# Performance work log

Hardware: AMD Instinct MI355X
Metric: run time of the kernel (lower is better)

The kernel has to match this reference:

```python
import jax, jax.numpy as jnp
import numpy as np

B, T, I, H, C = 8192, 28, 28, 128, 10


def setup_inputs() -> dict:
    key = jax.random.key(0)
    ks = jax.random.split(key, 7)
    s_ih = 1.0 / np.sqrt(H)
    return {
        "x": jax.random.normal(ks[0], (B, T, I), dtype=jnp.float32),
        "W_ih": jax.random.normal(ks[1], (4 * H, I), dtype=jnp.float32) * s_ih,
        "W_hh": jax.random.normal(ks[2], (4 * H, H), dtype=jnp.float32) * s_ih,
        "b_ih": jax.random.normal(ks[3], (4 * H,), dtype=jnp.float32) * s_ih,
        "b_hh": jax.random.normal(ks[4], (4 * H,), dtype=jnp.float32) * s_ih,
        "W_fc": jax.random.normal(ks[5], (C, H), dtype=jnp.float32) * s_ih,
        "b_fc": jnp.zeros((C,), dtype=jnp.float32),
    }


def reference(x, W_ih, W_hh, b_ih, b_hh, W_fc, b_fc):
    # x: [B, T, I]. PyTorch LSTM gate order: i, f, g, o.
    b = b_ih + b_hh  # [4H]
    # Precompute input projections for all timesteps: [T, B, 4H]
    x_proj = jnp.einsum("bti,gi->tbg", x, W_ih) + b
    h0 = jnp.zeros((x.shape[0], H), dtype=x.dtype)
    c0 = jnp.zeros_like(h0)

    def step(carry, xp_t):
        h, c = carry
        gates = xp_t + h @ W_hh.T  # [B, 4H]
        i_g, f_g, g_g, o_g = jnp.split(gates, 4, axis=-1)
        i_g = jax.nn.sigmoid(i_g)
        f_g = jax.nn.sigmoid(f_g)
        g_g = jnp.tanh(g_g)
        o_g = jax.nn.sigmoid(o_g)
        c = f_g * c + i_g * g_g
        h = o_g * jnp.tanh(c)
        return (h, c), None

    (h_last, _), _ = jax.lax.scan(step, (h0, c0), x_proj)
    # outputs[:, -1, :] == final hidden state; fc + relu
    return jax.nn.relu(h_last @ W_fc.T + b_fc)
```

## Files before the change

### kernel.cpp

```cpp
#include <hip/hip_runtime.h>
#include <math.h>

typedef __attribute__((ext_vector_type(8))) _Float16 half8;
typedef __attribute__((ext_vector_type(4))) _Float16 half4;
typedef __attribute__((ext_vector_type(4))) float    f32x4;
typedef __attribute__((ext_vector_type(2))) float    f32x2;

#define TSTEPS 28
#define IDIM   28
#define HDIM   128
#define NKC    5
#define TILE_B 32
#define CDIM   10

#if __has_builtin(__builtin_amdgcn_exp2f)
#define EXP2F(x) __builtin_amdgcn_exp2f(x)
#else
#define EXP2F(x) exp2f(x)
#endif
#if __has_builtin(__builtin_amdgcn_rcpf)
#define RCPF(x) __builtin_amdgcn_rcpf(x)
#else
#define RCPF(x) (1.0f / (x))
#endif
#if __has_builtin(__builtin_amdgcn_s_setprio)
#define SETPRIO(p) __builtin_amdgcn_s_setprio(p)
#else
#define SETPRIO(p)
#endif

#define NLOG2E (-1.44269504f)
#define P2LOG2E (2.88539008f)

#define MFMA16(a,b,c) __builtin_amdgcn_mfma_f32_16x16x32_f16((a),(b),(c),0,0,0)

__global__ __launch_bounds__(256) void pack_w(const float* __restrict__ Wih,
                                              const float* __restrict__ Whh,
                                              const float* __restrict__ bih,
                                              const float* __restrict__ bhh,
                                              _Float16* __restrict__ P) {
    int e = blockIdx.x * 256 + threadIdx.x;
    if (e >= NKC * 4 * 8 * 64 * 8) return;
    int j  = e & 7;
    int ln = (e >> 3) & 63;
    int w  = (e >> 9) & 7;
    int t  = (e >> 12) & 3;
    int kc = e >> 14;
    int k  = kc * 32 + ((ln >> 4) << 3) + j;
    int u  = w * 16 + (ln & 15);
    int g  = t * HDIM + u;
    float v = 0.f;
    if (k < HDIM)                   v = Whh[g * HDIM + k];
    else if (k < HDIM + IDIM)       v = Wih[g * IDIM + (k - HDIM)];
    else if (k == HDIM + IDIM)      v = bih[g] + bhh[g];
    float sc = (t == 2) ? P2LOG2E : NLOG2E;
    P[e] = (_Float16)(v * sc);
}

__global__ __launch_bounds__(512, 2) void lstm_kernel(
    const float* __restrict__ x,
    const _Float16* __restrict__ P,
    const float* __restrict__ Wfc,
    const float* __restrict__ b_fc,
    float* __restrict__ out)
{
    __shared__ __align__(16) _Float16 frag[2][NKC][64][8];
    __shared__ __align__(16) float hplain[TILE_B][HDIM + 4];

    const int tid = threadIdx.x;
    const int l   = tid & 63;
    const int w   = tid >> 6;
    const int sid = w >> 2;
    const int w4  = w & 3;
    const int b0  = blockIdx.x * TILE_B;

    half8 breg[4][2][4];
    half8 breg4[4][2];
    {
        const half8* Pp = (const half8*)P;
        #pragma unroll
        for (int g = 0; g < 4; ++g)
            #pragma unroll
            for (int n = 0; n < 2; ++n) {
                #pragma unroll
                for (int kc = 0; kc < 4; ++kc)
                    breg[g][n][kc] = Pp[((kc * 4 + g) * 8 + (2 * w4 + n)) * 64 + l];
                breg4[g][n] = Pp[((4 * 4 + g) * 8 + (2 * w4 + n)) * 64 + l];
            }
    }

    {
        float4 z = {0.f, 0.f, 0.f, 0.f};
        ((float4*)frag)[(tid < 256) ? tid : (tid + 64)] = z;
    }
    if (tid < 32) {
        int s = tid >> 4, i = tid & 15;
        half4 onev = {(_Float16)1.f, (_Float16)0.f, (_Float16)0.f, (_Float16)0.f};
        *(half4*)&frag[s][4][48 + i][4] = onev;
    }

    const int xid   = tid & 255;
    const bool xact = (xid < 112);
    const int xrow  = xid / 7, xg = xid % 7;
    const int xslot = xrow + 16 * (xg >> 1);
    const int xoff  = (xg & 1) * 4;
    const float4* xs4 = (const float4*)(x + (size_t)(b0 + sid * 16 + xrow) * (TSTEPS * IDIM));
    float4 xh;
    if (xact) {
        float4 x0 = xs4[xg];
        half4 h0 = {(_Float16)x0.x, (_Float16)x0.y, (_Float16)x0.z, (_Float16)x0.w};
        *(half4*)&frag[sid][4][xslot][xoff] = h0;
    }

    const int l15 = l & 15;
    const int mb  = (l >> 4) << 2;
    const int jh  = l & 7;
    const int q0  = (l >> 3) & 1;
    _Float16 (*myfrag)[64][8] = frag[sid];

    f32x4 acc[4][2];
    f32x2 cst[4];
    cst[0] = cst[1] = cst[2] = cst[3] = (f32x2){0.f, 0.f};
    const f32x4 zc = {0.f, 0.f, 0.f, 0.f};

    auto mfma_phase = [&](int t) {
        if (xact && t + 1 < TSTEPS) xh = xs4[(t + 1) * 7 + xg];
        half8 a0 = *(const half8*)&myfrag[0][l][0];
        half8 a1 = *(const half8*)&myfrag[1][l][0];
        half8 a2 = *(const half8*)&myfrag[2][l][0];
        half8 a3 = *(const half8*)&myfrag[3][l][0];
        half8 a4 = *(const half8*)&myfrag[4][l][0];
        SETPRIO(1);
        #pragma unroll
        for (int g = 0; g < 4; ++g)
            #pragma unroll
            for (int n = 0; n < 2; ++n) {
                f32x4 c = MFMA16(a4, breg4[g][n], zc);
                c = MFMA16(a0, breg[g][n][0], c);
                c = MFMA16(a1, breg[g][n][1], c);
                c = MFMA16(a2, breg[g][n][2], c);
                c = MFMA16(a3, breg[g][n][3], c);
                acc[g][n] = c;
            }
        SETPRIO(0);
    };

    auto act_phase = [&](int t) {
        const bool lastT = (t == TSTEPS - 1);
        #pragma unroll
        for (int n = 0; n < 2; ++n) {
            float hv[4];
            #pragma unroll
            for (int rp = 0; rp < 2; ++rp) {
                const int r0 = rp * 2, r1 = r0 + 1;
                f32x2 Ei = {EXP2F(acc[0][n][r0]), EXP2F(acc[0][n][r1])};
                f32x2 Ef = {EXP2F(acc[1][n][r0]), EXP2F(acc[1][n][r1])};
                f32x2 Eg = {EXP2F(acc[2][n][r0]), EXP2F(acc[2][n][r1])};
                f32x2 Eo = {EXP2F(acc[3][n][r0]), EXP2F(acc[3][n][r1])};
                f32x2 one = {1.f, 1.f};
                f32x2 Di = Ei + one, Df = Ef + one, Dg = Eg + one, Do = Eo + one;
                f32x2 Pif = Di * Df, Pgo = Dg * Do;
                f32x2 Rif = {RCPF(Pif.x), RCPF(Pif.y)};
                f32x2 Rgo = {RCPF(Pgo.x), RCPF(Pgo.y)};
                f32x2 is = Rif * Df, fs = Rif * Di;
                f32x2 gt = one - 2.f * (Rgo * Do);
                f32x2 os = Rgo * Dg;
                f32x2 c = fs * cst[2 * n + rp] + is * gt;
                cst[2 * n + rp] = c;
                f32x2 Etc = {EXP2F(c.x * P2LOG2E), EXP2F(c.y * P2LOG2E)};
                f32x2 Dtc = Etc + one;
                f32x2 Rtc = {RCPF(Dtc.x), RCPF(Dtc.y)};
                f32x2 tc = one - 2.f * Rtc;
                f32x2 h2 = os * tc;
                hv[r0] = h2.x; hv[r1] = h2.y;
            }
            if (lastT) {
                #pragma unroll
                for (int r = 0; r < 4; ++r)
                    hplain[sid * 16 + mb + r][32 * w4 + n * 16 + l15] = hv[r];
            } else {
                const int qn = q0 + 2 * n;
                #pragma unroll
                for (int r = 0; r < 4; ++r)
                    myfrag[w4][mb + r + 16 * qn][jh] = (_Float16)hv[r];
            }
        }
        if (xact && t + 1 < TSTEPS) {
            half4 hc = {(_Float16)xh.x, (_Float16)xh.y, (_Float16)xh.z, (_Float16)xh.w};
            *(half4*)&myfrag[4][xslot][xoff] = hc;
        }
    };

    __syncthreads();

    if (sid == 0) mfma_phase(0);
    __syncthreads();

    for (int t = 0; t < TSTEPS; ++t) {
        if (sid == 0) act_phase(t);
        else          mfma_phase(t);
        __syncthreads();
        if (sid == 0) { if (t + 1 < TSTEPS) mfma_phase(t + 1); }
        else          act_phase(t);
        __syncthreads();
    }

    if (tid < TILE_B * CDIM) {
        int row = tid / CDIM, c = tid % CDIM;
        const float4* hv4 = (const float4*)&hplain[row][0];
        const float4* wf  = (const float4*)(Wfc + c * HDIM);
        float s = b_fc[c];
        #pragma unroll
        for (int q = 0; q < 32; ++q) {
            float4 a4 = hv4[q], b4 = wf[q];
            s += a4.x * b4.x + a4.y * b4.y + a4.z * b4.z + a4.w * b4.w;
        }
        out[(size_t)(b0 + row) * CDIM + c] = fmaxf(s, 0.f);
    }
}

extern "C" void kernel_launch(void* const* d_in, const int* in_sizes, int n_in,
                              void* d_out, int out_size, void* d_ws, size_t ws_size,
                              hipStream_t stream) {
    const float* x   = (const float*)d_in[0];
    const float* Wih = (const float*)d_in[1];
    const float* Whh = (const float*)d_in[2];
    const float* bih = (const float*)d_in[3];
    const float* bhh = (const float*)d_in[4];
    const float* Wfc = (const float*)d_in[5];
    const float* bfc = (const float*)d_in[6];
    float* out = (float*)d_out;
    _Float16* P = (_Float16*)d_ws;

    hipLaunchKernelGGL(pack_w, dim3(320), dim3(256), 0, stream, Wih, Whh, bih, bhh, P);
    hipLaunchKernelGGL(lstm_kernel, dim3(8192 / TILE_B), dim3(512), 0, stream,
                       x, P, Wfc, bfc, out);
}
```

Measured before the change: 132.6 us.

## Double LSTM block to 1024 threads, one gate column group per wave

Each block now runs 16 waves instead of 8, so each wave computes one 16-unit hidden column group instead of two. This halves per-wave MFMA and activation work on the serial timestep critical path. The input/bias weight chunk moves from registers into LDS, and the MFMA chain is reordered so the four gate accumulators interleave. The cost is more LDS, extra LDS reads every step, and a (1024,4) launch bound that may force a very tight register budget and cause spills.

```diff
diff --git a/kernel.cpp b/kernel.cpp
--- a/kernel.cpp
+++ b/kernel.cpp
@@ -57,7 +57,7 @@
     P[e] = (_Float16)(v * sc);
 }
 
-__global__ __launch_bounds__(512, 2) void lstm_kernel(
+__global__ __launch_bounds__(1024, 4) void lstm_kernel(
     const float* __restrict__ x,
     const _Float16* __restrict__ P,
     const float* __restrict__ Wfc,
@@ -65,33 +65,36 @@
     float* __restrict__ out)
 {
     __shared__ __align__(16) _Float16 frag[2][NKC][64][8];
+    __shared__ __align__(16) _Float16 Plds[4][8][64][8];
     __shared__ __align__(16) float hplain[TILE_B][HDIM + 4];
 
     const int tid = threadIdx.x;
     const int l   = tid & 63;
     const int w   = tid >> 6;
-    const int sid = w >> 2;
-    const int w4  = w & 3;
+    const int sid = w >> 3;
+    const int w8  = w & 7;
     const int b0  = blockIdx.x * TILE_B;
 
-    half8 breg[4][2][4];
-    half8 breg4[4][2];
+    {
+        const float4* P4 = (const float4*)P;
+        float4* dst = (float4*)Plds;
+        dst[tid]        = P4[8192 + tid];
+        dst[tid + 1024] = P4[9216 + tid];
+    }
+    half8 breg[4][4];
     {
         const half8* Pp = (const half8*)P;
         #pragma unroll
-        for (int g = 0; g < 4; ++g)
+        for (int kc = 0; kc < 4; ++kc)
             #pragma unroll
-            for (int n = 0; n < 2; ++n) {
-                #pragma unroll
-                for (int kc = 0; kc < 4; ++kc)
-                    breg[g][n][kc] = Pp[((kc * 4 + g) * 8 + (2 * w4 + n)) * 64 + l];
-                breg4[g][n] = Pp[((4 * 4 + g) * 8 + (2 * w4 + n)) * 64 + l];
-            }
+            for (int g = 0; g < 4; ++g)
+                breg[g][kc] = Pp[((kc * 4 + g) * 8 + w8) * 64 + l];
     }
 
     {
         float4 z = {0.f, 0.f, 0.f, 0.f};
-        ((float4*)frag)[(tid < 256) ? tid : (tid + 64)] = z;
+        if (tid < 256)      ((float4*)frag)[tid] = z;
+        else if (tid < 512) ((float4*)frag)[tid + 64] = z;
     }
     if (tid < 32) {
         int s = tid >> 4, i = tid & 15;
@@ -99,9 +102,10 @@
         *(half4*)&frag[s][4][48 + i][4] = onev;
     }
 
-    const int xid   = tid & 255;
-    const bool xact = (xid < 112);
-    const int xrow  = xid / 7, xg = xid % 7;
+    const bool xact = (l < 14);
+    const int xid   = w8 * 14 + l;
+    const int xrow  = (xid / 7) & 15;
+    const int xg    = xid % 7;
     const int xslot = xrow + 16 * (xg >> 1);
     const int xoff  = (xg & 1) * 4;
     const float4* xs4 = (const float4*)(x + (size_t)(b0 + sid * 16 + xrow) * (TSTEPS * IDIM));
@@ -113,14 +117,15 @@
     }
 
     const int l15 = l & 15;
-    const int mb  = (l >> 4) << 2;
-    const int jh  = l & 7;
-    const int q0  = (l >> 3) & 1;
+    const int u    = w8 * 16 + l15;
+    const int kc_h = w8 >> 1;
+    const int quad = (2 * w8 + ((l >> 3) & 1)) & 3;
+    const int jh   = l & 7;
+    const int mb   = (l >> 4) << 2;
     _Float16 (*myfrag)[64][8] = frag[sid];
 
-    f32x4 acc[4][2];
-    f32x2 cst[4];
-    cst[0] = cst[1] = cst[2] = cst[3] = (f32x2){0.f, 0.f};
+    f32x4 acc[4];
+    f32x2 cst01 = {0.f, 0.f}, cst23 = {0.f, 0.f};
     const f32x4 zc = {0.f, 0.f, 0.f, 0.f};
 
     auto mfma_phase = [&](int t) {
@@ -132,58 +137,57 @@
         half8 a4 = *(const half8*)&myfrag[4][l][0];
         SETPRIO(1);
         #pragma unroll
-        for (int g = 0; g < 4; ++g)
-            #pragma unroll
-            for (int n = 0; n < 2; ++n) {
-                f32x4 c = MFMA16(a4, breg4[g][n], zc);
-                c = MFMA16(a0, breg[g][n][0], c);
-                c = MFMA16(a1, breg[g][n][1], c);
-                c = MFMA16(a2, breg[g][n][2], c);
-                c = MFMA16(a3, breg[g][n][3], c);
-                acc[g][n] = c;
-            }
+        for (int g = 0; g < 4; ++g) {
+            half8 pb = *(const half8*)&Plds[g][w8][l][0];
+            acc[g] = MFMA16(a4, pb, zc);
+        }
+        #pragma unroll
+        for (int g = 0; g < 4; ++g) acc[g] = MFMA16(a0, breg[g][0], acc[g]);
+        #pragma unroll
+        for (int g = 0; g < 4; ++g) acc[g] = MFMA16(a1, breg[g][1], acc[g]);
+        #pragma unroll
+        for (int g = 0; g < 4; ++g) acc[g] = MFMA16(a2, breg[g][2], acc[g]);
+        #pragma unroll
+        for (int g = 0; g < 4; ++g) acc[g] = MFMA16(a3, breg[g][3], acc[g]);
         SETPRIO(0);
     };
 
     auto act_phase = [&](int t) {
         const bool lastT = (t == TSTEPS - 1);
-        #pragma unroll
-        for (int n = 0; n < 2; ++n) {
-            float hv[4];
+        float hv[4];
+        #pragma unroll
+        for (int rp = 0; rp < 2; ++rp) {
+            const int r0 = rp * 2, r1 = r0 + 1;
+            f32x2 Ei = {EXP2F(acc[0][r0]), EXP2F(acc[0][r1])};
+            f32x2 Ef = {EXP2F(acc[1][r0]), EXP2F(acc[1][r1])};
+            f32x2 Eg = {EXP2F(acc[2][r0]), EXP2F(acc[2][r1])};
+            f32x2 Eo = {EXP2F(acc[3][r0]), EXP2F(acc[3][r1])};
+            f32x2 one = {1.f, 1.f};
+            f32x2 Di = Ei + one, Df = Ef + one, Dg = Eg + one, Do = Eo + one;
+            f32x2 Pif = Di * Df, Pgo = Dg * Do;
+            f32x2 Rif = {RCPF(Pif.x), RCPF(Pif.y)};
+            f32x2 Rgo = {RCPF(Pgo.x), RCPF(Pgo.y)};
+            f32x2 is = Rif * Df, fs = Rif * Di;
+            f32x2 gt = one - 2.f * (Rgo * Do);
+            f32x2 os = Rgo * Dg;
+            f32x2 cstp = rp ? cst23 : cst01;
+            f32x2 c = fs * cstp + is * gt;
+            if (rp) cst23 = c; else cst01 = c;
+            f32x2 Etc = {EXP2F(c.x * P2LOG2E), EXP2F(c.y * P2LOG2E)};
+            f32x2 Dtc = Etc + one;
+            f32x2 Rtc = {RCPF(Dtc.x), RCPF(Dtc.y)};
+            f32x2 tc = one - 2.f * Rtc;
+            f32x2 h2 = os * tc;
+            hv[r0] = h2.x; hv[r1] = h2.y;
+        }
+        if (lastT) {
             #pragma unroll
-            for (int rp = 0; rp < 2; ++rp) {
-                const int r0 = rp * 2, r1 = r0 + 1;
-                f32x2 Ei = {EXP2F(acc[0][n][r0]), EXP2F(acc[0][n][r1])};
-                f32x2 Ef = {EXP2F(acc[1][n][r0]), EXP2F(acc[1][n][r1])};
-                f32x2 Eg = {EXP2F(acc[2][n][r0]), EXP2F(acc[2][n][r1])};
-                f32x2 Eo = {EXP2F(acc[3][n][r0]), EXP2F(acc[3][n][r1])};
-                f32x2 one = {1.f, 1.f};
-                f32x2 Di = Ei + one, Df = Ef + one, Dg = Eg + one, Do = Eo + one;
-                f32x2 Pif = Di * Df, Pgo = Dg * Do;
-                f32x2 Rif = {RCPF(Pif.x), RCPF(Pif.y)};
-                f32x2 Rgo = {RCPF(Pgo.x), RCPF(Pgo.y)};
-                f32x2 is = Rif * Df, fs = Rif * Di;
-                f32x2 gt = one - 2.f * (Rgo * Do);
-                f32x2 os = Rgo * Dg;
-                f32x2 c = fs * cst[2 * n + rp] + is * gt;
-                cst[2 * n + rp] = c;
-                f32x2 Etc = {EXP2F(c.x * P2LOG2E), EXP2F(c.y * P2LOG2E)};
-                f32x2 Dtc = Etc + one;
-                f32x2 Rtc = {RCPF(Dtc.x), RCPF(Dtc.y)};
-                f32x2 tc = one - 2.f * Rtc;
-                f32x2 h2 = os * tc;
-                hv[r0] = h2.x; hv[r1] = h2.y;
-            }
-            if (lastT) {
-                #pragma unroll
-                for (int r = 0; r < 4; ++r)
-                    hplain[sid * 16 + mb + r][32 * w4 + n * 16 + l15] = hv[r];
-            } else {
-                const int qn = q0 + 2 * n;
-                #pragma unroll
-                for (int r = 0; r < 4; ++r)
-                    myfrag[w4][mb + r + 16 * qn][jh] = (_Float16)hv[r];
-            }
+            for (int r = 0; r < 4; ++r)
+                hplain[sid * 16 + mb + r][u] = hv[r];
+        } else {
+            #pragma unroll
+            for (int r = 0; r < 4; ++r)
+                myfrag[kc_h][mb + r + 16 * quad][jh] = (_Float16)hv[r];
         }
         if (xact && t + 1 < TSTEPS) {
             half4 hc = {(_Float16)xh.x, (_Float16)xh.y, (_Float16)xh.z, (_Float16)xh.w};
@@ -233,6 +237,6 @@
     _Float16* P = (_Float16*)d_ws;
 
     hipLaunchKernelGGL(pack_w, dim3(320), dim3(256), 0, stream, Wih, Whh, bih, bhh, P);
-    hipLaunchKernelGGL(lstm_kernel, dim3(8192 / TILE_B), dim3(512), 0, stream,
+    hipLaunchKernelGGL(lstm_kernel, dim3(8192 / TILE_B), dim3(1024), 0, stream,
                        x, P, Wfc, bfc, out);
 }
```

After: 137.3 us. 1.03x slower.
